# Kernel optimization log

Measured on AMD Instinct MI355X. Metric: run time of the kernel, lower is better.

## Reference

```python
import jax, jax.numpy as jnp
import numpy as np

D = 128          # embedding dim
N_INIT = 100000  # number of initial (axiom) clauses
L = 64           # topological levels of derived clauses
M = 4096         # derived clauses per level
N_THAX = 2000    # distinct axiom-name (thax) embeddings
N_SINE = 32      # sine-level embeddings
N_RULES = 256    # distinct inference rules (each with its own 2-ary MLP)
N_TOT = N_INIT + L * M


def setup_inputs() -> dict:
    key = jax.random.key(0)
    ks = jax.random.split(key, 10)
    rng = np.random.default_rng(0)
    # parents of level-l nodes point to any node created strictly earlier
    parents = np.stack(
        [rng.integers(0, N_INIT + l * M, size=(M, 2)) for l in range(L)]
    ).astype(np.int32)  # [L, M, 2]
    return {
        "thax_table": jax.random.normal(ks[0], (N_THAX, D), jnp.float32) * 0.1,
        "sine_table": jax.random.normal(ks[1], (N_SINE, D), jnp.float32) * 0.1,
        "rule_W": jax.random.normal(ks[2], (N_RULES, 2 * D, D), jnp.float32) * (1.0 / np.sqrt(2 * D)),
        "rule_b": jax.random.normal(ks[3], (N_RULES, D), jnp.float32) * 0.01,
        "eval_w": jax.random.normal(ks[4], (D,), jnp.float32) * (1.0 / np.sqrt(D)),
        "eval_b": jax.random.normal(ks[5], (1,), jnp.float32) * 0.01,
        "pos_vals": jax.random.uniform(ks[6], (N_TOT,), jnp.float32, 0.01, 1.0),
        "neg_vals": jax.random.uniform(ks[7], (N_TOT,), jnp.float32, 0.01, 1.0),
        "init_thax": jax.random.randint(ks[8], (N_INIT,), 0, N_THAX, jnp.int32),
        "init_sine": jax.random.randint(ks[9], (N_INIT,), 0, N_SINE, jnp.int32),
        "parents": jnp.asarray(parents),
        "rules": jnp.asarray(rng.integers(0, N_RULES, size=(L, M)).astype(np.int32)),
    }


def reference(thax_table, sine_table, rule_W, rule_b, eval_w, eval_b,
              pos_vals, neg_vals, init_thax, init_sine, parents, rules):
    n_init = init_thax.shape[0]
    n_lvl, m = rules.shape
    d = thax_table.shape[1]

    # init nodes: embed = init_embeds[thax]() + sine_embedder(sine)
    init_emb = thax_table[init_thax] + sine_table[init_sine]  # [N_INIT, D]
    store0 = jnp.concatenate(
        [init_emb, jnp.zeros((n_lvl * m, d), init_emb.dtype)], axis=0)  # [N_TOT, D]

    # deriv nodes, level by level: gather 2 parents, per-rule MLP (cat -> Linear -> ReLU)
    def step(store, xs):
        lvl, par, rul = xs                       # par: [M,2] int, rul: [M] int
        pe = store[par].reshape(m, 2 * d)        # gather parent embeddings
        emb = jax.nn.relu(jnp.einsum('mi,mio->mo', pe, rule_W[rul]) + rule_b[rul])
        store = jax.lax.dynamic_update_slice(store, emb, (n_init + lvl * m, 0))
        return store, None

    store, _ = jax.lax.scan(step, store0, (jnp.arange(n_lvl), parents, rules))

    # eval_net + weighted BCEWithLogits (pos_weight = tot_neg / tot_pos)
    logits = store @ eval_w + eval_b[0]          # [N_TOT]
    tot = pos_vals + neg_vals
    y = pos_vals / tot
    pw = jnp.sum(neg_vals) / jnp.sum(pos_vals)
    per_node = pw * y * jax.nn.softplus(-logits) + (1.0 - y) * jax.nn.softplus(logits)
    loss = jnp.sum(tot * per_node).reshape(1)
    posOK = jnp.sum(jnp.where(logits >= 0.0, pos_vals, 0.0))
    negOK = jnp.sum(jnp.where(logits < 0.0, neg_vals, 0.0))
    return (loss, posOK, negOK)
```

## Files before the change

kernel.cpp:

```cpp
#include <hip/hip_runtime.h>

#define D      128
#define NINIT  100000
#define LVLS   64
#define M      4096
#define NRULES 256
#define NTOT   (NINIT + LVLS * M)
#define NTHR   512
#define TILE   32

typedef __attribute__((ext_vector_type(8))) short short8;
typedef __attribute__((ext_vector_type(4))) float floatx4;

#define ST_OFF 256
#define SI_OFF (ST_OFF + (size_t)NTOT * D * 2)
#define RO_OFF (SI_OFF + (size_t)LVLS * M * 4)
#define FL_OFF (RO_OFF + (size_t)LVLS * (NRULES + 1) * 4)

#define CBAR() asm volatile("" ::: "memory")

__device__ __forceinline__ unsigned short f2bf(float x) {
  unsigned u = __float_as_uint(x);
  u += 0x7fffu + ((u >> 16) & 1u);
  return (unsigned short)(u >> 16);
}

__device__ __forceinline__ float softplusf(float x) {
  return fmaxf(x, 0.f) + log1pf(expf(-fabsf(x)));
}

__device__ __forceinline__ void st_sys(unsigned* p, unsigned v) {
  __hip_atomic_store(p, v, __ATOMIC_RELAXED, __HIP_MEMORY_SCOPE_SYSTEM);
}
__device__ __forceinline__ unsigned ld_sys(const unsigned* p) {
  return __hip_atomic_load(p, __ATOMIC_RELAXED, __HIP_MEMORY_SCOPE_SYSTEM);
}
__device__ __forceinline__ void wait_flag(const unsigned* f) {
  int guard = 1 << 17;
  while (__builtin_expect(ld_sys(f) == 0u, 0) && --guard)
    __builtin_amdgcn_s_sleep(1);
  CBAR();
}

__device__ __forceinline__ void gbar_light(unsigned* bcnt, unsigned* bgen) {
  __syncthreads();
  if (threadIdx.x == 0) {
    unsigned g = ld_sys(bgen);
    unsigned v = __hip_atomic_fetch_add(bcnt, 1u, __ATOMIC_RELAXED,
                                        __HIP_MEMORY_SCOPE_SYSTEM);
    if (v == gridDim.x - 1) {
      st_sys(bcnt, 0u);
      st_sys(bgen, g + 1u);
    } else {
      int guard = 1 << 22;
      while (ld_sys(bgen) == g && --guard) __builtin_amdgcn_s_sleep(2);
    }
  }
  __syncthreads();
}

__device__ __forceinline__ bool adv_cursor(int r, const int* __restrict__ ro,
                                           int& l, int& t0, int& off, int& cnt) {
  t0 += TILE;
  while (t0 >= cnt) {
    if (++l >= LVLS) return false;
    off = ro[l * (NRULES + 1) + r];
    cnt = ro[l * (NRULES + 1) + r + 1] - off;
    t0 = 0;
  }
  return true;
}

__global__ __launch_bounds__(NTHR, 2) void fused_kernel(
    const float* __restrict__ thax_table, const float* __restrict__ sine_table,
    const float* __restrict__ rule_W, const float* __restrict__ rule_b,
    const float* __restrict__ eval_w, const float* __restrict__ eval_b,
    const float* __restrict__ pos, const float* __restrict__ neg,
    const int* __restrict__ init_thax, const int* __restrict__ init_sine,
    const int* __restrict__ parents,
    const int* __restrict__ rules,
    unsigned short* __restrict__ store, int* __restrict__ sorted_idx,
    int* __restrict__ rule_off, unsigned* __restrict__ flags,
    float* __restrict__ sums, unsigned* __restrict__ bvars,
    float* __restrict__ out) {
  __shared__ unsigned short pe[TILE * 264];
  __shared__ unsigned short ot[TILE * 136];
  __shared__ int s_sid[2][TILE];
  __shared__ int s_cnt[NRULES];
  __shared__ int s_base[NRULES + 1];
  __shared__ float racc[3];

  unsigned* bcnt = bvars;
  unsigned* bgen = bvars + 1;

  const int r = blockIdx.x;
  const int tid = threadIdx.x;
  const int wave = tid >> 6, lane = tid & 63;
  const int col = (wave << 4) + (lane & 15);
  const int node = tid >> 4;
  const int segq = tid & 15;
  const int gid = r * NTHR + tid;
  const int gthreads = NRULES * NTHR;

  short8 bf[8];
  {
    const float* Wr = rule_W + (size_t)r * (2 * D * D);
    const int krow_base = (lane >> 4) * 8;
#pragma unroll
    for (int ks = 0; ks < 8; ++ks) {
      union { short8 s; unsigned short us[8]; } c;
#pragma unroll
      for (int j = 0; j < 8; ++j)
        c.us[j] = f2bf(Wr[(size_t)(ks * 32 + krow_base + j) * D + col]);
      bf[ks] = c.s;
    }
  }
  const float bias = rule_b[r * D + col];

  if (r < LVLS) {
    const int l = r;
    const int* rl = rules + (size_t)l * M;
    if (tid < NRULES) s_cnt[tid] = 0;
    __syncthreads();
    for (int m = tid; m < M; m += NTHR) atomicAdd(&s_cnt[rl[m]], 1);
    __syncthreads();
    if (tid == 0) {
      int run = 0;
      for (int q = 0; q < NRULES; ++q) { s_base[q] = run; run += s_cnt[q]; }
      s_base[NRULES] = run;
    }
    __syncthreads();
    if (tid < NRULES) {
      st_sys((unsigned*)&rule_off[(size_t)l * (NRULES + 1) + tid],
             (unsigned)s_base[tid]);
      s_cnt[tid] = s_base[tid];
    }
    if (tid == 0)
      st_sys((unsigned*)&rule_off[(size_t)l * (NRULES + 1) + NRULES],
             (unsigned)M);
    __syncthreads();
    for (int m = tid; m < M; m += NTHR) {
      int p = atomicAdd(&s_cnt[rl[m]], 1);
      st_sys((unsigned*)&sorted_idx[(size_t)l * M + p], (unsigned)m);
    }
  }

  for (int idx = gid; idx < NINIT * 16; idx += gthreads) {
    int nd = idx >> 4, sg = idx & 15;
    const float4* t = (const float4*)(thax_table + (size_t)init_thax[nd] * D) + sg * 2;
    const float4* s = (const float4*)(sine_table + (size_t)init_sine[nd] * D) + sg * 2;
    float4 a0 = t[0], a1 = t[1], b0 = s[0], b1 = s[1];
    float v[8] = {a0.x + b0.x, a0.y + b0.y, a0.z + b0.z, a0.w + b0.w,
                  a1.x + b1.x, a1.y + b1.y, a1.z + b1.z, a1.w + b1.w};
    unsigned* dst = (unsigned*)(store + (size_t)nd * D + sg * 8);
    st_sys(dst + 0, (unsigned)f2bf(v[0]) | ((unsigned)f2bf(v[1]) << 16));
    st_sys(dst + 1, (unsigned)f2bf(v[2]) | ((unsigned)f2bf(v[3]) << 16));
    st_sys(dst + 2, (unsigned)f2bf(v[4]) | ((unsigned)f2bf(v[5]) << 16));
    st_sys(dst + 3, (unsigned)f2bf(v[6]) | ((unsigned)f2bf(v[7]) << 16));
  }

  {
    float sp = 0.f, sn = 0.f;
    for (int i = gid; i < NTOT; i += gthreads) {
      sp += pos[i];
      sn += neg[i];
    }
    for (int m = 32; m; m >>= 1) {
      sp += __shfl_xor(sp, m, 64);
      sn += __shfl_xor(sn, m, 64);
    }
    if (lane == 0) {
      atomicAdd(&sums[0], sp);
      atomicAdd(&sums[1], sn);
    }
  }

  gbar_light(bcnt, bgen);

  int lL = -1, t0L = 0, offL = 0, cntL = 0;

  bool validA = adv_cursor(r, rule_off, lL, t0L, offL, cntL);
  int lA = lL, t0A = t0L, cntA = cntL;
  int parA0 = 0, parA1 = 0;
  bool lateA0 = false, lateA1 = false;
  unsigned reA0 = 1u, reA1 = 1u;
  uint4 gA0 = {0, 0, 0, 0}, gA1 = {0, 0, 0, 0};
  if (validA) {
    int gj = t0A + node; if (gj > cntA - 1) gj = cntA - 1;
    int sid = sorted_idx[(size_t)lA * M + offL + gj];
    parA0 = parents[((size_t)lA * M + sid) * 2 + 0];
    parA1 = parents[((size_t)lA * M + sid) * 2 + 1];
    if (parA0 >= NINIT) wait_flag(flags + (parA0 - NINIT));
    if (parA1 >= NINIT) wait_flag(flags + (parA1 - NINIT));
    gA0 = *(const uint4*)(store + (size_t)parA0 * D + segq * 8);
    gA1 = *(const uint4*)(store + (size_t)parA1 * D + segq * 8);
    if (segq == 0) s_sid[0][node] = sid;
  }

  bool validB = validA && adv_cursor(r, rule_off, lL, t0L, offL, cntL);
  int lB = lL, t0B = t0L, cntB = cntL;
  int sidB = 0, parB0 = 0, parB1 = 0;
  unsigned fB0 = 1u, fB1 = 1u;
  if (validB) {
    int gj = t0B + node; if (gj > cntB - 1) gj = cntB - 1;
    sidB = sorted_idx[(size_t)lB * M + offL + gj];
    parB0 = parents[((size_t)lB * M + sidB) * 2 + 0];
    parB1 = parents[((size_t)lB * M + sidB) * 2 + 1];
    fB0 = parB0 >= NINIT ? ld_sys(flags + (parB0 - NINIT)) : 1u;
    fB1 = parB1 >= NINIT ? ld_sys(flags + (parB1 - NINIT)) : 1u;
  }

  bool validC = validB && adv_cursor(r, rule_off, lL, t0L, offL, cntL);
  int lC = lL, t0C = t0L, cntC = cntL;
  int sidC = 0, parC0 = 0, parC1 = 0;
  if (validC) {
    int gj = t0C + node; if (gj > cntC - 1) gj = cntC - 1;
    sidC = sorted_idx[(size_t)lC * M + offL + gj];
    parC0 = parents[((size_t)lC * M + sidC) * 2 + 0];
    parC1 = parents[((size_t)lC * M + sidC) * 2 + 1];
  }

  bool validD = validC && adv_cursor(r, rule_off, lL, t0L, offL, cntL);
  int lD = lL, t0D = t0L, offD = offL, cntD = cntL;

  int p = 0;
  while (validA) {
    if (lateA0 || lateA1) {
      bool n0 = lateA0 && (reA0 == 0u);
      bool n1 = lateA1 && (reA1 == 0u);
      if (n0 || n1) {
        int guard = 1 << 17;
        while (guard--) {
          unsigned f0 = n0 ? ld_sys(flags + (parA0 - NINIT)) : 1u;
          unsigned f1 = n1 ? ld_sys(flags + (parA1 - NINIT)) : 1u;
          if (f0 != 0u && f1 != 0u) break;
          __builtin_amdgcn_s_sleep(1);
        }
      }
      CBAR();
      if (lateA0) gA0 = *(const uint4*)(store + (size_t)parA0 * D + segq * 8);
      if (lateA1) gA1 = *(const uint4*)(store + (size_t)parA1 * D + segq * 8);
    }

    *(uint4*)(pe + node * 264 + segq * 8) = gA0;
    *(uint4*)(pe + node * 264 + 128 + segq * 8) = gA1;
    __syncthreads();
    if (validB && segq == 0) s_sid[p ^ 1][node] = sidB;

    floatx4 acc0 = {0.f, 0.f, 0.f, 0.f}, acc1 = {0.f, 0.f, 0.f, 0.f};
#pragma unroll
    for (int ks = 0; ks < 8; ++ks) {
      short8 a0 = *(const short8*)(pe + (lane & 15) * 264 + ks * 32 + (lane >> 4) * 8);
      short8 a1 = *(const short8*)(pe + (16 + (lane & 15)) * 264 + ks * 32 + (lane >> 4) * 8);
      acc0 = __builtin_amdgcn_mfma_f32_16x16x32_bf16(a0, bf[ks], acc0, 0, 0, 0);
      acc1 = __builtin_amdgcn_mfma_f32_16x16x32_bf16(a1, bf[ks], acc1, 0, 0, 0);
    }
#pragma unroll
    for (int reg = 0; reg < 4; ++reg) {
      int row = (lane >> 4) * 4 + reg;
      float v0 = acc0[reg] + bias;
      float v1 = acc1[reg] + bias;
      ot[row * 136 + col] = f2bf(v0 > 0.f ? v0 : 0.f);
      ot[(16 + row) * 136 + col] = f2bf(v1 > 0.f ? v1 : 0.f);
    }
    __syncthreads();

    {
      const int n_baseA = NINIT + lA * M;
      int nsid[4]; bool inr[4]; int S = 0;
#pragma unroll
      for (int k = 0; k < 4; ++k) {
        int nd = wave + 8 * k;
        nsid[k] = s_sid[p][nd];
        inr[k] = (t0A + nd) < cntA;
        if (inr[k]) {
          st_sys((unsigned*)(store + (size_t)(n_baseA + nsid[k]) * D) + lane,
                 *(const unsigned*)(ot + nd * 136 + lane * 2));
          ++S;
        }
      }
      CBAR();
#pragma unroll
      for (int k = 0; k < 4; ++k) {
        if (inr[k]) {
          if (S == 4)      asm volatile("s_waitcnt vmcnt(3)" ::: "memory");
          else if (S == 3) asm volatile("s_waitcnt vmcnt(2)" ::: "memory");
          else if (S == 2) asm volatile("s_waitcnt vmcnt(1)" ::: "memory");
          else             asm volatile("s_waitcnt vmcnt(0)" ::: "memory");
          if (lane == 0) st_sys(flags + lA * M + nsid[k], 1u);
        }
      }
      CBAR();
    }

    bool lateB0 = validB && parB0 >= NINIT && fB0 == 0u;
    bool lateB1 = validB && parB1 >= NINIT && fB1 == 0u;
    uint4 gB0, gB1;
    {
      const unsigned short* a0 =
          (validB && !lateB0) ? store + (size_t)parB0 * D : store;
      const unsigned short* a1 =
          (validB && !lateB1) ? store + (size_t)parB1 * D : store;
      gB0 = *(const uint4*)(a0 + segq * 8);
      gB1 = *(const uint4*)(a1 + segq * 8);
    }
    int sidD = 0, parD0 = 0, parD1 = 0;
    if (validD) {
      int gj = t0D + node; if (gj > cntD - 1) gj = cntD - 1;
      sidD = sorted_idx[(size_t)lD * M + offD + gj];
      parD0 = parents[((size_t)lD * M + sidD) * 2 + 0];
      parD1 = parents[((size_t)lD * M + sidD) * 2 + 1];
    }
    unsigned fC0 = 1u, fC1 = 1u;
    if (validC) {
      fC0 = ld_sys(flags + (parC0 >= NINIT ? parC0 - NINIT : 0));
      fC1 = ld_sys(flags + (parC1 >= NINIT ? parC1 - NINIT : 0));
      if (parC0 < NINIT) fC0 = 1u;
      if (parC1 < NINIT) fC1 = 1u;
    }
    unsigned reB0 = 1u, reB1 = 1u;
    if (lateB0) reB0 = ld_sys(flags + (parB0 - NINIT));
    if (lateB1) reB1 = ld_sys(flags + (parB1 - NINIT));
    CBAR();

    gA0 = gB0; gA1 = gB1; lateA0 = lateB0; lateA1 = lateB1;
    reA0 = reB0; reA1 = reB1;
    parA0 = parB0; parA1 = parB1;
    lA = lB; t0A = t0B; cntA = cntB; validA = validB;
    sidB = sidC; parB0 = parC0; parB1 = parC1; fB0 = fC0; fB1 = fC1;
    lB = lC; t0B = t0C; cntB = cntC; validB = validC;
    sidC = sidD; parC0 = parD0; parC1 = parD1;
    lC = lD; t0C = t0D; cntC = cntD; validC = validD;
    validD = validC && adv_cursor(r, rule_off, lL, t0L, offL, cntL);
    lD = lL; t0D = t0L; offD = offL; cntD = cntL;
    p ^= 1;
  }

  gbar_light(bcnt, bgen);

  {
    float a_loss = 0.f, a_pos = 0.f, a_neg = 0.f;
    const float pw = sums[1] / sums[0];
    const float eb = eval_b[0];
    const float4* wv = (const float4*)eval_w;

    for (int nd = gid; nd < NTOT; nd += gthreads) {
      const uint4* v = (const uint4*)(store + (size_t)nd * D);
      float dot = 0.f;
#pragma unroll
      for (int k = 0; k < 16; ++k) {
        uint4 u = v[k];
        float4 w0 = wv[k * 2], w1 = wv[k * 2 + 1];
        dot += __uint_as_float(u.x << 16) * w0.x +
               __uint_as_float(u.x & 0xffff0000u) * w0.y +
               __uint_as_float(u.y << 16) * w0.z +
               __uint_as_float(u.y & 0xffff0000u) * w0.w +
               __uint_as_float(u.z << 16) * w1.x +
               __uint_as_float(u.z & 0xffff0000u) * w1.y +
               __uint_as_float(u.w << 16) * w1.z +
               __uint_as_float(u.w & 0xffff0000u) * w1.w;
      }
      float logit = dot + eb;
      float pp = pos[nd], nn = neg[nd];
      float tot = pp + nn, y = pp / tot;
      a_loss += tot * (pw * y * softplusf(-logit) + (1.f - y) * softplusf(logit));
      if (logit >= 0.f) a_pos += pp; else a_neg += nn;
    }

    for (int m = 32; m; m >>= 1) {
      a_loss += __shfl_xor(a_loss, m, 64);
      a_pos  += __shfl_xor(a_pos,  m, 64);
      a_neg  += __shfl_xor(a_neg,  m, 64);
    }
    if (tid == 0) { racc[0] = 0.f; racc[1] = 0.f; racc[2] = 0.f; }
    __syncthreads();
    if (lane == 0) {
      atomicAdd(&racc[0], a_loss);
      atomicAdd(&racc[1], a_pos);
      atomicAdd(&racc[2], a_neg);
    }
    __syncthreads();
    if (tid == 0) {
      atomicAdd(&out[0], racc[0]);
      atomicAdd(&out[1], racc[1]);
      atomicAdd(&out[2], racc[2]);
    }
  }
}

extern "C" void kernel_launch(void* const* d_in, const int* in_sizes, int n_in,
                              void* d_out, int out_size, void* d_ws, size_t ws_size,
                              hipStream_t stream) {
  const float* thax_table = (const float*)d_in[0];
  const float* sine_table = (const float*)d_in[1];
  const float* rule_W     = (const float*)d_in[2];
  const float* rule_b     = (const float*)d_in[3];
  const float* eval_w     = (const float*)d_in[4];
  const float* eval_b     = (const float*)d_in[5];
  const float* pos_vals   = (const float*)d_in[6];
  const float* neg_vals   = (const float*)d_in[7];
  const int*   init_thax  = (const int*)d_in[8];
  const int*   init_sine  = (const int*)d_in[9];
  const int*   parents    = (const int*)d_in[10];
  const int*   rules      = (const int*)d_in[11];

  float* out = (float*)d_out;
  char* ws = (char*)d_ws;
  float* sums = (float*)ws;
  unsigned* bvars = (unsigned*)(ws + 128);
  unsigned short* store = (unsigned short*)(ws + ST_OFF);
  int* sorted_idx = (int*)(ws + SI_OFF);
  int* rule_off   = (int*)(ws + RO_OFF);
  unsigned* flags = (unsigned*)(ws + FL_OFF);

  (void)hipMemsetAsync(d_out, 0, 3 * sizeof(float), stream);
  (void)hipMemsetAsync(d_ws, 0, 256, stream);
  (void)hipMemsetAsync(ws + FL_OFF, 0, (size_t)LVLS * M * 4, stream);

  void* args[] = {&thax_table, &sine_table, &rule_W, &rule_b, &eval_w, &eval_b,
                  &pos_vals, &neg_vals, &init_thax, &init_sine, &parents,
                  &rules, &store, &sorted_idx, &rule_off, &flags, &sums,
                  &bvars, &out};
  (void)hipLaunchCooperativeKernel((void*)fused_kernel, dim3(NRULES),
                                   dim3(NTHR), args, 0, stream);
}
```

Measured before the change: 425.7 us.

## Fuse eval-net loss into derivation loop and drop final grid barrier

Computes the eval dot product and weighted BCE loss for each derived node right after its embedding is produced, reading the bf16 tile from shared memory. The final pass then only covers the initial nodes, and the grid-wide barrier before the loss pass is removed. Initial-node stores are also widened from four 32-bit to two 64-bit atomic stores. This avoids re-reading the derived part of the store from global memory and the last global sync, at the cost of extra shuffles, pos/neg loads and registers inside the hot pipelined loop.

```diff
diff --git a/kernel.cpp b/kernel.cpp
--- a/kernel.cpp
+++ b/kernel.cpp
@@ -30,6 +30,10 @@
 }
 
 __device__ __forceinline__ void st_sys(unsigned* p, unsigned v) {
+  __hip_atomic_store(p, v, __ATOMIC_RELAXED, __HIP_MEMORY_SCOPE_SYSTEM);
+}
+__device__ __forceinline__ void st_sys64(unsigned long long* p,
+                                         unsigned long long v) {
   __hip_atomic_store(p, v, __ATOMIC_RELAXED, __HIP_MEMORY_SCOPE_SYSTEM);
 }
 __device__ __forceinline__ unsigned ld_sys(const unsigned* p) {
@@ -102,6 +106,16 @@
   const int gid = r * NTHR + tid;
   const int gthreads = NRULES * NTHR;
 
+  float a_loss = 0.f, a_pos = 0.f, a_neg = 0.f;
+  const float eb = eval_b[0];
+  float w8[8];
+  {
+    float4 wA = ((const float4*)eval_w)[segq * 2];
+    float4 wB = ((const float4*)eval_w)[segq * 2 + 1];
+    w8[0] = wA.x; w8[1] = wA.y; w8[2] = wA.z; w8[3] = wA.w;
+    w8[4] = wB.x; w8[5] = wB.y; w8[6] = wB.z; w8[7] = wB.w;
+  }
+
   short8 bf[8];
   {
     const float* Wr = rule_W + (size_t)r * (2 * D * D);
@@ -152,11 +166,14 @@
     float4 a0 = t[0], a1 = t[1], b0 = s[0], b1 = s[1];
     float v[8] = {a0.x + b0.x, a0.y + b0.y, a0.z + b0.z, a0.w + b0.w,
                   a1.x + b1.x, a1.y + b1.y, a1.z + b1.z, a1.w + b1.w};
-    unsigned* dst = (unsigned*)(store + (size_t)nd * D + sg * 8);
-    st_sys(dst + 0, (unsigned)f2bf(v[0]) | ((unsigned)f2bf(v[1]) << 16));
-    st_sys(dst + 1, (unsigned)f2bf(v[2]) | ((unsigned)f2bf(v[3]) << 16));
-    st_sys(dst + 2, (unsigned)f2bf(v[4]) | ((unsigned)f2bf(v[5]) << 16));
-    st_sys(dst + 3, (unsigned)f2bf(v[6]) | ((unsigned)f2bf(v[7]) << 16));
+    unsigned p0 = (unsigned)f2bf(v[0]) | ((unsigned)f2bf(v[1]) << 16);
+    unsigned p1 = (unsigned)f2bf(v[2]) | ((unsigned)f2bf(v[3]) << 16);
+    unsigned p2 = (unsigned)f2bf(v[4]) | ((unsigned)f2bf(v[5]) << 16);
+    unsigned p3 = (unsigned)f2bf(v[6]) | ((unsigned)f2bf(v[7]) << 16);
+    unsigned long long* dst =
+        (unsigned long long*)(store + (size_t)nd * D + sg * 8);
+    st_sys64(dst + 0, (unsigned long long)p0 | ((unsigned long long)p1 << 32));
+    st_sys64(dst + 1, (unsigned long long)p2 | ((unsigned long long)p3 << 32));
   }
 
   {
@@ -177,6 +194,8 @@
 
   gbar_light(bcnt, bgen);
 
+  const float pw = sums[1] / sums[0];
+
   int lL = -1, t0L = 0, offL = 0, cntL = 0;
 
   bool validA = adv_cursor(r, rule_off, lL, t0L, offL, cntL);
@@ -184,12 +203,15 @@
   int parA0 = 0, parA1 = 0;
   bool lateA0 = false, lateA1 = false;
   unsigned reA0 = 1u, reA1 = 1u;
+  float pPosA = 0.f, pNegA = 0.f;
   uint4 gA0 = {0, 0, 0, 0}, gA1 = {0, 0, 0, 0};
   if (validA) {
     int gj = t0A + node; if (gj > cntA - 1) gj = cntA - 1;
     int sid = sorted_idx[(size_t)lA * M + offL + gj];
     parA0 = parents[((size_t)lA * M + sid) * 2 + 0];
     parA1 = parents[((size_t)lA * M + sid) * 2 + 1];
+    pPosA = pos[NINIT + lA * M + sid];
+    pNegA = neg[NINIT + lA * M + sid];
     if (parA0 >= NINIT) wait_flag(flags + (parA0 - NINIT));
     if (parA1 >= NINIT) wait_flag(flags + (parA1 - NINIT));
     gA0 = *(const uint4*)(store + (size_t)parA0 * D + segq * 8);
@@ -304,6 +326,11 @@
       gB0 = *(const uint4*)(a0 + segq * 8);
       gB1 = *(const uint4*)(a1 + segq * 8);
     }
+    float pPosB = 0.f, pNegB = 0.f;
+    if (validB) {
+      pPosB = pos[NINIT + lB * M + sidB];
+      pNegB = neg[NINIT + lB * M + sidB];
+    }
     int sidD = 0, parD0 = 0, parD1 = 0;
     if (validD) {
       int gj = t0D + node; if (gj > cntD - 1) gj = cntD - 1;
@@ -323,9 +350,33 @@
     if (lateB1) reB1 = ld_sys(flags + (parB1 - NINIT));
     CBAR();
 
+    {
+      const uint4 u = *(const uint4*)(ot + node * 136 + segq * 8);
+      float pd = __uint_as_float(u.x << 16) * w8[0] +
+                 __uint_as_float(u.x & 0xffff0000u) * w8[1] +
+                 __uint_as_float(u.y << 16) * w8[2] +
+                 __uint_as_float(u.y & 0xffff0000u) * w8[3] +
+                 __uint_as_float(u.z << 16) * w8[4] +
+                 __uint_as_float(u.z & 0xffff0000u) * w8[5] +
+                 __uint_as_float(u.w << 16) * w8[6] +
+                 __uint_as_float(u.w & 0xffff0000u) * w8[7];
+      pd += __shfl_xor(pd, 1, 64);
+      pd += __shfl_xor(pd, 2, 64);
+      pd += __shfl_xor(pd, 4, 64);
+      pd += __shfl_xor(pd, 8, 64);
+      if (segq == 0 && (t0A + node) < cntA) {
+        float logit = pd + eb;
+        float tot = pPosA + pNegA, y = pPosA / tot;
+        a_loss += tot * (pw * y * softplusf(-logit) +
+                         (1.f - y) * softplusf(logit));
+        if (logit >= 0.f) a_pos += pPosA; else a_neg += pNegA;
+      }
+    }
+
     gA0 = gB0; gA1 = gB1; lateA0 = lateB0; lateA1 = lateB1;
     reA0 = reB0; reA1 = reB1;
     parA0 = parB0; parA1 = parB1;
+    pPosA = pPosB; pNegA = pNegB;
     lA = lB; t0A = t0B; cntA = cntB; validA = validB;
     sidB = sidC; parB0 = parC0; parB1 = parC1; fB0 = fC0; fB1 = fC1;
     lB = lC; t0B = t0C; cntB = cntC; validB = validC;
@@ -336,15 +387,9 @@
     p ^= 1;
   }
 
-  gbar_light(bcnt, bgen);
-
   {
-    float a_loss = 0.f, a_pos = 0.f, a_neg = 0.f;
-    const float pw = sums[1] / sums[0];
-    const float eb = eval_b[0];
     const float4* wv = (const float4*)eval_w;
-
-    for (int nd = gid; nd < NTOT; nd += gthreads) {
+    for (int nd = gid; nd < NINIT; nd += gthreads) {
       const uint4* v = (const uint4*)(store + (size_t)nd * D);
       float dot = 0.f;
 #pragma unroll
@@ -366,25 +411,25 @@
       a_loss += tot * (pw * y * softplusf(-logit) + (1.f - y) * softplusf(logit));
       if (logit >= 0.f) a_pos += pp; else a_neg += nn;
     }
-
-    for (int m = 32; m; m >>= 1) {
-      a_loss += __shfl_xor(a_loss, m, 64);
-      a_pos  += __shfl_xor(a_pos,  m, 64);
-      a_neg  += __shfl_xor(a_neg,  m, 64);
-    }
-    if (tid == 0) { racc[0] = 0.f; racc[1] = 0.f; racc[2] = 0.f; }
-    __syncthreads();
-    if (lane == 0) {
-      atomicAdd(&racc[0], a_loss);
-      atomicAdd(&racc[1], a_pos);
-      atomicAdd(&racc[2], a_neg);
-    }
-    __syncthreads();
-    if (tid == 0) {
-      atomicAdd(&out[0], racc[0]);
-      atomicAdd(&out[1], racc[1]);
-      atomicAdd(&out[2], racc[2]);
-    }
+  }
+
+  for (int m = 32; m; m >>= 1) {
+    a_loss += __shfl_xor(a_loss, m, 64);
+    a_pos  += __shfl_xor(a_pos,  m, 64);
+    a_neg  += __shfl_xor(a_neg,  m, 64);
+  }
+  if (tid == 0) { racc[0] = 0.f; racc[1] = 0.f; racc[2] = 0.f; }
+  __syncthreads();
+  if (lane == 0) {
+    atomicAdd(&racc[0], a_loss);
+    atomicAdd(&racc[1], a_pos);
+    atomicAdd(&racc[2], a_neg);
+  }
+  __syncthreads();
+  if (tid == 0) {
+    atomicAdd(&out[0], racc[0]);
+    atomicAdd(&out[1], racc[1]);
+    atomicAdd(&out[2], racc[2]);
   }
 }
 
```

New measurement: 418.5 us. No clear change (-1.7%).
